# Optimization experiments

Hardware: AMD Instinct MI355X
Metric: run time of the kernel (lower is better)

The kernel has to match this reference:

```python
import jax, jax.numpy as jnp
import numpy as np

# Model hyperparameters (hardcoded in GarNetClassificationModel.__init__)
N_BLOCKS, N_AGG, N_FILT, N_PROP = 11, 4, 32, 20
B, V, F_IN = 128, 1024, 10
D_GEX = 2 * F_IN                                   # after GlobalExchange concat
D_UPD = N_FILT + N_AGG * 2 * (N_PROP + N_AGG) + N_AGG  # 32 + 192 + 4 = 228
BN_EPS = 1e-3                                      # keras BatchNormalization default


def setup_inputs() -> dict:
    key = jax.random.key(0)
    ks = iter(jax.random.split(key, 32))
    n = lambda shape, s=0.1: jax.random.normal(next(ks), shape, jnp.float32) * s
    return dict(
        x=jax.random.normal(next(ks), (B, V, F_IN), jnp.float32),
        bn0_gamma=jnp.ones((D_GEX,), jnp.float32),
        bn0_beta=jnp.zeros((D_GEX,), jnp.float32),
        bn0_mean=n((D_GEX,)),
        bn0_var=jax.random.uniform(next(ks), (D_GEX,), jnp.float32, 0.5, 1.5),
        W_in=n((D_GEX, N_FILT), 0.3),
        b_in=jnp.zeros((N_FILT,), jnp.float32),
        W_flr=n((N_BLOCKS, N_FILT, N_PROP), 0.2),
        b_flr=jnp.zeros((N_BLOCKS, N_PROP), jnp.float32),
        W_s=n((N_BLOCKS, N_FILT, N_AGG), 0.2),
        b_s=jnp.zeros((N_BLOCKS, N_AGG), jnp.float32),
        W_out=n((N_BLOCKS, D_UPD, N_FILT), 0.1),
        b_out=jnp.zeros((N_BLOCKS, N_FILT), jnp.float32),
        bn_gamma=jnp.ones((N_BLOCKS, N_FILT), jnp.float32),
        bn_beta=jnp.zeros((N_BLOCKS, N_FILT), jnp.float32),
        bn_mean=n((N_BLOCKS, N_FILT)),
        bn_var=jax.random.uniform(next(ks), (N_BLOCKS, N_FILT), jnp.float32, 0.5, 1.5),
        W_o0=n((N_BLOCKS * N_FILT, 48), 0.1),
        b_o0=jnp.zeros((48,), jnp.float32),
        W_o1=n((48, 3), 0.2),
        b_o1=jnp.zeros((3,), jnp.float32),
    )


def _bn(x, g, b, m, v):
    # inference-mode BatchNormalization over last axis
    return (x - m) * (g * jax.lax.rsqrt(v + BN_EPS)) + b


def reference(x, bn0_gamma, bn0_beta, bn0_mean, bn0_var, W_in, b_in,
              W_flr, b_flr, W_s, b_s, W_out, b_out,
              bn_gamma, bn_beta, bn_mean, bn_var,
              W_o0, b_o0, W_o1, b_o1):
    # GlobalExchange: concat per-event mean over vertices to each vertex
    mean = jnp.mean(x, axis=1, keepdims=True)                   # (B,1,F)
    h = jnp.concatenate([x, jnp.broadcast_to(mean, x.shape)], axis=-1)  # (B,V,2F)
    h = _bn(h, bn0_gamma, bn0_beta, bn0_mean, bn0_var)
    h = jnp.tanh(h @ W_in + b_in)                               # (B,V,32)

    def block(h, p):
        Wf, bf, Ws, bs, Wo, bo, g, be, m, v = p
        f = h @ Wf + bf                                  # (B,V,P) propagate features
        d = h @ Ws + bs                                  # (B,V,A) aggregator distances
        w = jnp.exp(-jnp.abs(d))                         # (B,V,A) edge weights
        feat = jnp.concatenate([f, w], axis=-1)          # (B,V,P+A)
        wf = w[..., None] * feat[:, :, None, :]          # (B,V,A,P+A)
        agg = jnp.concatenate([wf.max(axis=1), wf.mean(axis=1)], axis=-1)  # (B,A,2(P+A))
        upd = (w[..., None] * agg[:, None, :, :]).reshape(h.shape[0], h.shape[1], -1)  # (B,V,A*2(P+A))
        out = jnp.tanh(jnp.concatenate([h, upd, w], axis=-1) @ Wo + bo)  # (B,V,32)
        out = _bn(out, g, be, m, v)
        return out, out

    params = (W_flr, b_flr, W_s, b_s, W_out, b_out, bn_gamma, bn_beta, bn_mean, bn_var)
    _, feats = jax.lax.scan(block, h, params)            # feats: (L,B,V,32)
    feats = jnp.moveaxis(feats, 0, 2).reshape(x.shape[0], x.shape[1], -1)  # (B,V,L*32)

    h = jax.nn.relu(feats @ W_o0 + b_o0)                 # (B,V,48)
    return jax.nn.relu(h @ W_o1 + b_o1)                  # (B,V,3)
```

## Files before the change

### kernel.cpp

```cpp
#include <hip/hip_runtime.h>
#include <math.h>

#define NBLK  11
#define NAGG  4
#define NFILT 32
#define NPROP 20
#define BB    128
#define VV    1024
#define HV    512
#define FIN   10
#define TPB   512
#define BN_EPS 1e-3f
#define SHS   40

#define WSF_MEAN 128
#define WSF_AGG  (WSF_MEAN + BB*2*FIN)
#define WSF_FRAG (WSF_AGG + (BB*2*2) * NAGG * 48)
#define NFRAG    (NBLK*7*64*8)

typedef _Float16 f16;
typedef f16   f16x8 __attribute__((ext_vector_type(8)));
typedef float f32x4 __attribute__((ext_vector_type(4)));

__device__ __forceinline__ f32x4 MFMA(f16x8 a, f16x8 b, f32x4 c){
  return __builtin_amdgcn_mfma_f32_16x16x32_f16(a, b, c, 0, 0, 0);
}

__device__ __forceinline__ float fast_tanh(float x){
  float a = fabsf(x);
  float e = __expf(-2.0f * a);
  float r = (1.0f - e) / (1.0f + e);
  return copysignf(r, x);
}

__device__ __forceinline__ void pair_sync(int* flag, int target){
  __syncthreads();
  if (threadIdx.x == 0){
    asm volatile("s_waitcnt vmcnt(0)" ::: "memory");
    __hip_atomic_fetch_add(flag, 1, __ATOMIC_RELAXED, __HIP_MEMORY_SCOPE_AGENT);
    while (__hip_atomic_load(flag, __ATOMIC_RELAXED, __HIP_MEMORY_SCOPE_AGENT) < target)
      __builtin_amdgcn_s_sleep(2);
  }
  __syncthreads();
}

extern "C" __global__ void garnet_prep(
    const float* __restrict__ W_flr, const float* __restrict__ W_s,
    const float* __restrict__ W_out, const float* __restrict__ W_o0,
    f16* __restrict__ frag)
{
  const int idx = blockIdx.x * blockDim.x + threadIdx.x;
  if (idx >= NFRAG) return;
  const int j    = idx & 7;
  const int lane = (idx >> 3) & 63;
  const int rest = idx >> 9;
  const int set  = rest % 7;
  const int l    = rest / 7;
  const int l16  = lane & 15, kb = lane >> 4, k = kb*8 + j;
  float val = 0.f;
  if (set < 2){
    const int n = set*16 + l16;
    if (set == 0) val = W_flr[l*NFILT*NPROP + k*NPROP + n];
    else          val = (n < 20) ? W_flr[l*NFILT*NPROP + k*NPROP + n]
                       : (n < 24 ? W_s[l*NFILT*NAGG + k*NAGG + (n-20)] : 0.f);
  } else if (set < 4){
    const int s = set - 2;
    val = W_out[l*228*NFILT + k*NFILT + s*16 + l16];
  } else {
    const int s = set - 4;
    val = W_o0[((size_t)l*NFILT + k)*48 + s*16 + l16];
  }
  frag[idx] = (f16)val;
}

extern "C" __global__ __launch_bounds__(TPB)
void garnet_fused(
    const float* __restrict__ x,
    const float* __restrict__ bn0_g, const float* __restrict__ bn0_b,
    const float* __restrict__ bn0_m, const float* __restrict__ bn0_v,
    const float* __restrict__ W_in,  const float* __restrict__ b_in,
    const float* __restrict__ W_flr, const float* __restrict__ b_flr,
    const float* __restrict__ W_s,   const float* __restrict__ b_s,
    const float* __restrict__ W_out, const float* __restrict__ b_out,
    const float* __restrict__ bn_g,  const float* __restrict__ bn_b,
    const float* __restrict__ bn_m,  const float* __restrict__ bn_v,
    const float* __restrict__ W_o0,  const float* __restrict__ b_o0,
    const float* __restrict__ W_o1,  const float* __restrict__ b_o1,
    int* __restrict__ wsFlag, float* __restrict__ wsF,
    const f16* __restrict__ frag,
    float* __restrict__ out)
{
  const int wg   = blockIdx.x;
  const int b    = wg & (BB - 1);
  const int half = wg >> 7;
  const int t    = threadIdx.x;
  const int lane = t & 63;
  const int wave = t >> 6;
  const int v    = half * HV + t;
  const int l16  = lane & 15;
  const int kb   = lane >> 4;

  __shared__ float sFeat[HV * 25];
  __shared__ __align__(16) f16 sHhi[HV * SHS];
  __shared__ __align__(16) f16 sHlo[HV * SHS];
  __shared__ f16   sMh[4 * 32];
  __shared__ float sAgg[NAGG][48];
  __shared__ float sRed[8][FIN];
  __shared__ float sMean[FIN];

  int* flag = wsFlag + b;

  {
    float h[NFILT];
    float xv[FIN];
    const float* xp = x + ((size_t)b * VV + v) * FIN;
    #pragma unroll
    for (int c = 0; c < FIN; ++c) xv[c] = xp[c];

    float ps[FIN];
    #pragma unroll
    for (int c = 0; c < FIN; ++c) ps[c] = xv[c];
    #pragma unroll
    for (int m = 32; m > 0; m >>= 1){
      #pragma unroll
      for (int c = 0; c < FIN; ++c) ps[c] += __shfl_xor(ps[c], m, 64);
    }
    if (lane == 0){
      #pragma unroll
      for (int c = 0; c < FIN; ++c) sRed[wave][c] = ps[c];
    }
    __syncthreads();
    if (t < FIN){
      float s = 0.f;
      #pragma unroll
      for (int wv = 0; wv < 8; ++wv) s += sRed[wv][t];
      sRed[0][t] = s;
      __hip_atomic_store(&wsF[WSF_MEAN + (b*2 + half)*FIN + t], s,
                         __ATOMIC_RELAXED, __HIP_MEMORY_SCOPE_AGENT);
    }
    pair_sync(flag, 2);
    if (t < FIN){
      float theirs = __hip_atomic_load(&wsF[WSF_MEAN + (b*2 + (half^1))*FIN + t],
                                       __ATOMIC_RELAXED, __HIP_MEMORY_SCOPE_AGENT);
      sMean[t] = (sRed[0][t] + theirs) * (1.0f / VV);
    }
    __syncthreads();

    float o[NFILT];
    #pragma unroll
    for (int j = 0; j < NFILT; ++j) o[j] = b_in[j];
    #pragma unroll
    for (int c = 0; c < FIN; ++c){
      const float zx = (xv[c]    - bn0_m[c])     * (bn0_g[c]     * rsqrtf(bn0_v[c]     + BN_EPS)) + bn0_b[c];
      const float zm = (sMean[c] - bn0_m[FIN+c]) * (bn0_g[FIN+c] * rsqrtf(bn0_v[FIN+c] + BN_EPS)) + bn0_b[FIN+c];
      #pragma unroll
      for (int j = 0; j < NFILT; ++j)
        o[j] += zx * W_in[c*NFILT + j] + zm * W_in[(FIN+c)*NFILT + j];
    }
    #pragma unroll
    for (int j = 0; j < NFILT; ++j) h[j] = fast_tanh(o[j]);

    #pragma unroll
    for (int c = 0; c < 4; ++c){
      f16x8 hh, hl;
      #pragma unroll
      for (int j = 0; j < 8; ++j){
        const float hv = h[c*8 + j];
        const f16 a = (f16)hv;
        hh[j] = a;
        hl[j] = (f16)(hv - (float)a);
      }
      *(f16x8*)&sHhi[t*SHS + c*8] = hh;
      *(f16x8*)&sHlo[t*SHS + c*8] = hl;
    }
  }
  __syncthreads();

  f32x4 acc[4][3];
  #pragma unroll
  for (int s = 0; s < 3; ++s){
    const float a0 = b_o0[s*16 + l16];
    #pragma unroll
    for (int i = 0; i < 4; ++i) acc[i][s] = (f32x4){a0, a0, a0, a0};
  }

  for (int l = 0; l < NBLK; ++l){
    const float* Wf = W_flr + l * NFILT * NPROP;
    const float* bf = b_flr + l * NPROP;
    const float* Ws = W_s   + l * NFILT * NAGG;
    const float* bs = b_s   + l * NAGG;
    const float* Wo = W_out + l * 228 * NFILT;
    const float* bo = b_out + l * NFILT;
    const float* g_ = bn_g  + l * NFILT;
    const float* be = bn_b  + l * NFILT;
    const float* bm = bn_m  + l * NFILT;
    const float* bv = bn_v  + l * NFILT;
    const f16*  fl  = frag + (size_t)l * 7 * 64 * 8;

    {
      f16x8 b1f0, b1f1;
      if (frag){
        b1f0 = *(const f16x8*)&fl[(size_t)(0*64 + lane)*8];
        b1f1 = *(const f16x8*)&fl[(size_t)(1*64 + lane)*8];
      } else {
        #pragma unroll
        for (int j = 0; j < 8; ++j){
          const int k = kb*8 + j;
          b1f0[j] = (f16)Wf[k*NPROP + l16];
          const int n = 16 + l16;
          b1f1[j] = (f16)((n < 20) ? Wf[k*NPROP + n] : (n < 24 ? Ws[k*NAGG + (n-20)] : 0.f));
        }
      }
      const float bias0 = bf[l16];
      const int  c1 = 16 + l16;
      const float bias1 = (c1 < 20) ? bf[c1] : (c1 < 24 ? bs[c1-20] : 0.f);

      #pragma unroll
      for (int i = 0; i < 4; ++i){
        const int tb = wave*64 + i*16;
        const f16x8 ahi = *(const f16x8*)&sHhi[(tb + l16)*SHS + kb*8];
        const f16x8 alo = *(const f16x8*)&sHlo[(tb + l16)*SHS + kb*8];
        f32x4 c0 = (f32x4){bias0, bias0, bias0, bias0};
        c0 = MFMA(ahi, b1f0, c0);
        c0 = MFMA(alo, b1f0, c0);
        #pragma unroll
        for (int q = 0; q < 4; ++q)
          sFeat[(tb + kb*4 + q)*25 + l16] = c0[q];
        f32x4 c1v = (f32x4){bias1, bias1, bias1, bias1};
        c1v = MFMA(ahi, b1f1, c1v);
        c1v = MFMA(alo, b1f1, c1v);
        if (l16 < 4){
          #pragma unroll
          for (int q = 0; q < 4; ++q)
            sFeat[(tb + kb*4 + q)*25 + 16 + l16] = c1v[q];
        } else if (l16 < 8){
          #pragma unroll
          for (int q = 0; q < 4; ++q)
            sFeat[(tb + kb*4 + q)*25 + 16 + l16] = __expf(-fabsf(c1v[q]));
        }
      }
    }
    __syncthreads();

    {
      const int w3 = wave * 3;
      float psum[NAGG][3], pmax[NAGG][3];
      #pragma unroll
      for (int a = 0; a < NAGG; ++a)
        #pragma unroll
        for (int c = 0; c < 3; ++c){ psum[a][c] = 0.f; pmax[a][c] = -INFINITY; }
      for (int i = 0; i < 8; ++i){
        const int row = i * 64 + lane;
        float fc[3], wa[NAGG];
        #pragma unroll
        for (int c = 0; c < 3; ++c) fc[c] = sFeat[row*25 + w3 + c];
        #pragma unroll
        for (int a = 0; a < NAGG; ++a) wa[a] = sFeat[row*25 + NPROP + a];
        #pragma unroll
        for (int a = 0; a < NAGG; ++a)
          #pragma unroll
          for (int c = 0; c < 3; ++c){
            const float p = wa[a] * fc[c];
            psum[a][c] += p;
            pmax[a][c]  = fmaxf(pmax[a][c], p);
          }
      }
      #pragma unroll
      for (int m = 32; m > 0; m >>= 1){
        #pragma unroll
        for (int a = 0; a < NAGG; ++a)
          #pragma unroll
          for (int c = 0; c < 3; ++c){
            psum[a][c] += __shfl_xor(psum[a][c], m, 64);
            pmax[a][c]  = fmaxf(pmax[a][c], __shfl_xor(pmax[a][c], m, 64));
          }
      }
      if (lane == 0){
        float* gp = wsF + WSF_AGG + (((size_t)(b*2 + (l&1))*2 + half) * NAGG * 48);
        #pragma unroll
        for (int a = 0; a < NAGG; ++a)
          #pragma unroll
          for (int c = 0; c < 3; ++c){
            sAgg[a][w3 + c]      = pmax[a][c];
            sAgg[a][24 + w3 + c] = psum[a][c];
            __hip_atomic_store(&gp[a*48 + w3 + c],      pmax[a][c], __ATOMIC_RELAXED, __HIP_MEMORY_SCOPE_AGENT);
            __hip_atomic_store(&gp[a*48 + 24 + w3 + c], psum[a][c], __ATOMIC_RELAXED, __HIP_MEMORY_SCOPE_AGENT);
          }
      }
    }
    pair_sync(flag, 2*l + 4);

    if (t < 192){
      const int a = t / 48, c = t - a * 48;
      const float* pp = wsF + WSF_AGG + (((size_t)(b*2 + (l&1))*2 + (half^1)) * NAGG * 48);
      const float mine   = sAgg[a][c];
      const float theirs = __hip_atomic_load(&pp[a*48 + c], __ATOMIC_RELAXED, __HIP_MEMORY_SCOPE_AGENT);
      sAgg[a][c] = (c < 24) ? fmaxf(mine, theirs) : (mine + theirs) * (1.0f / VV);
    }
    __syncthreads();

    if (t < 128){
      const int a = t >> 5, j = t & 31;
      float m = Wo[(224 + a) * NFILT + j];
      #pragma unroll 8
      for (int c = 0; c < 48; ++c) m += sAgg[a][c] * Wo[(32 + a*48 + c) * NFILT + j];
      sMh[a*32 + j] = (f16)m;
    }
    __syncthreads();

    {
      f16x8 b2f0, b2f1;
      if (frag){
        b2f0 = *(const f16x8*)&fl[(size_t)(2*64 + lane)*8];
        b2f1 = *(const f16x8*)&fl[(size_t)(3*64 + lane)*8];
      } else {
        #pragma unroll
        for (int j = 0; j < 8; ++j){
          const int k = kb*8 + j;
          b2f0[j] = (f16)Wo[k*NFILT + l16];
          b2f1[j] = (f16)Wo[k*NFILT + 16 + l16];
        }
      }
      f16x8 bmf[2];
      #pragma unroll
      for (int s = 0; s < 2; ++s)
        #pragma unroll
        for (int j = 0; j < 8; ++j)
          bmf[s][j] = (kb == 0 && j < 4) ? sMh[j*32 + s*16 + l16] : (f16)0.f;

      float boc[2], bmc[2], scc[2], bec[2];
      #pragma unroll
      for (int s = 0; s < 2; ++s){
        const int cc = s*16 + l16;
        boc[s] = bo[cc];
        bmc[s] = bm[cc];
        scc[s] = g_[cc] * rsqrtf(bv[cc] + BN_EPS);
        bec[s] = be[cc];
      }

      #pragma unroll
      for (int i = 0; i < 4; ++i){
        const int tb = wave*64 + i*16;
        const f16x8 ahi = *(const f16x8*)&sHhi[(tb + l16)*SHS + kb*8];
        const f16x8 alo = *(const f16x8*)&sHlo[(tb + l16)*SHS + kb*8];
        f16x8 wa;
        #pragma unroll
        for (int j = 0; j < 8; ++j) wa[j] = (f16)0.f;
        {
          const float w0 = sFeat[(tb + l16)*25 + 20];
          const float w1 = sFeat[(tb + l16)*25 + 21];
          const float w2 = sFeat[(tb + l16)*25 + 22];
          const float w3v = sFeat[(tb + l16)*25 + 23];
          if (kb == 0){ wa[0]=(f16)w0; wa[1]=(f16)w1; wa[2]=(f16)w2; wa[3]=(f16)w3v; }
        }
        #pragma unroll
        for (int s = 0; s < 2; ++s){
          f32x4 o = (f32x4){0.f, 0.f, 0.f, 0.f};
          o = MFMA(ahi, (s ? b2f1 : b2f0), o);
          o = MFMA(alo, (s ? b2f1 : b2f0), o);
          o = MFMA(wa,  bmf[s], o);
          #pragma unroll
          for (int q = 0; q < 4; ++q){
            const float th = fast_tanh(o[q] + boc[s]);
            const float hn = (th - bmc[s]) * scc[s] + bec[s];
            const f16 hh = (f16)hn;
            const int idx = (tb + kb*4 + q)*SHS + s*16 + l16;
            sHhi[idx] = hh;
            sHlo[idx] = (f16)(hn - (float)hh);
          }
        }
      }
    }
    asm volatile("s_waitcnt lgkmcnt(0)" ::: "memory");

    {
      f16x8 b3f[3];
      if (frag){
        #pragma unroll
        for (int s = 0; s < 3; ++s)
          b3f[s] = *(const f16x8*)&fl[(size_t)((4 + s)*64 + lane)*8];
      } else {
        const float* Wo0l = W_o0 + (size_t)l * NFILT * 48;
        #pragma unroll
        for (int s = 0; s < 3; ++s)
          #pragma unroll
          for (int j = 0; j < 8; ++j)
            b3f[s][j] = (f16)Wo0l[(kb*8 + j)*48 + s*16 + l16];
      }
      #pragma unroll
      for (int i = 0; i < 4; ++i){
        const int tb = wave*64 + i*16;
        const f16x8 ahi = *(const f16x8*)&sHhi[(tb + l16)*SHS + kb*8];
        const f16x8 alo = *(const f16x8*)&sHlo[(tb + l16)*SHS + kb*8];
        #pragma unroll
        for (int s = 0; s < 3; ++s){
          acc[i][s] = MFMA(ahi, b3f[s], acc[i][s]);
          acc[i][s] = MFMA(alo, b3f[s], acc[i][s]);
        }
      }
    }
  }

  {
    float w1c[3][3];
    #pragma unroll
    for (int s = 0; s < 3; ++s)
      #pragma unroll
      for (int m = 0; m < 3; ++m) w1c[s][m] = W_o1[(s*16 + l16)*3 + m];
    const float bo1_0 = b_o1[0], bo1_1 = b_o1[1], bo1_2 = b_o1[2];

    #pragma unroll
    for (int i = 0; i < 4; ++i){
      const int tb = wave*64 + i*16;
      float p[4][3];
      #pragma unroll
      for (int q = 0; q < 4; ++q){ p[q][0]=0.f; p[q][1]=0.f; p[q][2]=0.f; }
      #pragma unroll
      for (int s = 0; s < 3; ++s)
        #pragma unroll
        for (int q = 0; q < 4; ++q){
          const float r_ = fmaxf(acc[i][s][q], 0.f);
          p[q][0] += r_ * w1c[s][0];
          p[q][1] += r_ * w1c[s][1];
          p[q][2] += r_ * w1c[s][2];
        }
      #pragma unroll
      for (int m = 1; m <= 8; m <<= 1)
        #pragma unroll
        for (int q = 0; q < 4; ++q){
          p[q][0] += __shfl_xor(p[q][0], m, 64);
          p[q][1] += __shfl_xor(p[q][1], m, 64);
          p[q][2] += __shfl_xor(p[q][2], m, 64);
        }
      if (l16 < 3){
        const float bo1v = (l16 == 0) ? bo1_0 : ((l16 == 1) ? bo1_1 : bo1_2);
        #pragma unroll
        for (int q = 0; q < 4; ++q){
          const float vv = (l16 == 0) ? p[q][0] : ((l16 == 1) ? p[q][1] : p[q][2]);
          out[((size_t)b*VV + half*HV + tb + kb*4 + q)*3 + l16] = fmaxf(vv + bo1v, 0.f);
        }
      }
    }
  }
}

extern "C" void kernel_launch(void* const* d_in, const int* in_sizes, int n_in,
                              void* d_out, int out_size, void* d_ws, size_t ws_size,
                              hipStream_t stream) {
  const float* x      = (const float*)d_in[0];
  const float* bn0_g  = (const float*)d_in[1];
  const float* bn0_b  = (const float*)d_in[2];
  const float* bn0_m  = (const float*)d_in[3];
  const float* bn0_v  = (const float*)d_in[4];
  const float* W_in   = (const float*)d_in[5];
  const float* b_in   = (const float*)d_in[6];
  const float* W_flr  = (const float*)d_in[7];
  const float* b_flr  = (const float*)d_in[8];
  const float* W_s    = (const float*)d_in[9];
  const float* b_s    = (const float*)d_in[10];
  const float* W_out  = (const float*)d_in[11];
  const float* b_out  = (const float*)d_in[12];
  const float* bn_g   = (const float*)d_in[13];
  const float* bn_b   = (const float*)d_in[14];
  const float* bn_m   = (const float*)d_in[15];
  const float* bn_v   = (const float*)d_in[16];
  const float* W_o0   = (const float*)d_in[17];
  const float* b_o0   = (const float*)d_in[18];
  const float* W_o1   = (const float*)d_in[19];
  const float* b_o1   = (const float*)d_in[20];

  float* wsF = (float*)d_ws;
  const size_t needed = (size_t)WSF_FRAG * 4 + (size_t)NFRAG * 2;
  _Float16* frag = (ws_size >= needed) ? (_Float16*)(wsF + WSF_FRAG) : nullptr;

  hipMemsetAsync(d_ws, 0, BB * sizeof(int), stream);

  if (frag)
    garnet_prep<<<dim3((NFRAG + 255) / 256), dim3(256), 0, stream>>>(
        W_flr, W_s, W_out, W_o0, frag);

  garnet_fused<<<dim3(BB * 2), dim3(TPB), 0, stream>>>(
      x, bn0_g, bn0_b, bn0_m, bn0_v, W_in, b_in,
      W_flr, b_flr, W_s, b_s, W_out, b_out,
      bn_g, bn_b, bn_m, bn_v, W_o0, b_o0, W_o1, b_o1,
      (int*)d_ws, wsF, frag, (float*)d_out);
}
```

Baseline: 164.1 us.

## Overlap previous block's output projection with cross-workgroup sync wait; transpose feature buffer

The per-block W_o0 accumulation (phaseC) for layer l-1 is deferred and run between the atomic flag increment and the spin-wait on the partner workgroup, so the MFMA work hides the inter-workgroup barrier latency. The final layer's accumulation moves after the loop. The sFeat buffer is also transposed to a feature-major layout with padded stride, enabling vectorized f32x4 stores and conflict-free column reads. This relies on sHhi/sHlo still holding layer l-1's hidden state during the wait, which holds because the update phase runs after the sync.

```diff
diff --git a/kernel.cpp b/kernel.cpp
--- a/kernel.cpp
+++ b/kernel.cpp
@@ -12,6 +12,7 @@
 #define TPB   512
 #define BN_EPS 1e-3f
 #define SHS   40
+#define SFS   536
 
 #define WSF_MEAN 128
 #define WSF_AGG  (WSF_MEAN + BB*2*FIN)
@@ -31,17 +32,6 @@
   float e = __expf(-2.0f * a);
   float r = (1.0f - e) / (1.0f + e);
   return copysignf(r, x);
-}
-
-__device__ __forceinline__ void pair_sync(int* flag, int target){
-  __syncthreads();
-  if (threadIdx.x == 0){
-    asm volatile("s_waitcnt vmcnt(0)" ::: "memory");
-    __hip_atomic_fetch_add(flag, 1, __ATOMIC_RELAXED, __HIP_MEMORY_SCOPE_AGENT);
-    while (__hip_atomic_load(flag, __ATOMIC_RELAXED, __HIP_MEMORY_SCOPE_AGENT) < target)
-      __builtin_amdgcn_s_sleep(2);
-  }
-  __syncthreads();
 }
 
 extern "C" __global__ void garnet_prep(
@@ -100,7 +90,7 @@
   const int l16  = lane & 15;
   const int kb   = lane >> 4;
 
-  __shared__ float sFeat[HV * 25];
+  __shared__ float sFeatT[24 * SFS];
   __shared__ __align__(16) f16 sHhi[HV * SHS];
   __shared__ __align__(16) f16 sHlo[HV * SHS];
   __shared__ f16   sMh[4 * 32];
@@ -110,6 +100,36 @@
 
   int* flag = wsFlag + b;
 
+  f32x4 acc[4][3];
+
+  auto phaseC = [&](int lc){
+    f16x8 b3f[3];
+    if (frag){
+      const f16* flC = frag + (size_t)lc * 7 * 64 * 8;
+      #pragma unroll
+      for (int s = 0; s < 3; ++s)
+        b3f[s] = *(const f16x8*)&flC[(size_t)((4 + s)*64 + lane)*8];
+    } else {
+      const float* Wo0l = W_o0 + (size_t)lc * NFILT * 48;
+      #pragma unroll
+      for (int s = 0; s < 3; ++s)
+        #pragma unroll
+        for (int j = 0; j < 8; ++j)
+          b3f[s][j] = (f16)Wo0l[(kb*8 + j)*48 + s*16 + l16];
+    }
+    #pragma unroll
+    for (int i = 0; i < 4; ++i){
+      const int tb = wave*64 + i*16;
+      const f16x8 ahi = *(const f16x8*)&sHhi[(tb + l16)*SHS + kb*8];
+      const f16x8 alo = *(const f16x8*)&sHlo[(tb + l16)*SHS + kb*8];
+      #pragma unroll
+      for (int s = 0; s < 3; ++s){
+        acc[i][s] = MFMA(ahi, b3f[s], acc[i][s]);
+        acc[i][s] = MFMA(alo, b3f[s], acc[i][s]);
+      }
+    }
+  };
+
   {
     float h[NFILT];
     float xv[FIN];
@@ -138,7 +158,14 @@
       __hip_atomic_store(&wsF[WSF_MEAN + (b*2 + half)*FIN + t], s,
                          __ATOMIC_RELAXED, __HIP_MEMORY_SCOPE_AGENT);
     }
-    pair_sync(flag, 2);
+    __syncthreads();
+    if (t == 0){
+      asm volatile("s_waitcnt vmcnt(0)" ::: "memory");
+      __hip_atomic_fetch_add(flag, 1, __ATOMIC_RELAXED, __HIP_MEMORY_SCOPE_AGENT);
+      while (__hip_atomic_load(flag, __ATOMIC_RELAXED, __HIP_MEMORY_SCOPE_AGENT) < 2)
+        __builtin_amdgcn_s_sleep(2);
+    }
+    __syncthreads();
     if (t < FIN){
       float theirs = __hip_atomic_load(&wsF[WSF_MEAN + (b*2 + (half^1))*FIN + t],
                                        __ATOMIC_RELAXED, __HIP_MEMORY_SCOPE_AGENT);
@@ -176,7 +203,6 @@
   }
   __syncthreads();
 
-  f32x4 acc[4][3];
   #pragma unroll
   for (int s = 0; s < 3; ++s){
     const float a0 = b_o0[s*16 + l16];
@@ -223,20 +249,17 @@
         f32x4 c0 = (f32x4){bias0, bias0, bias0, bias0};
         c0 = MFMA(ahi, b1f0, c0);
         c0 = MFMA(alo, b1f0, c0);
-        #pragma unroll
-        for (int q = 0; q < 4; ++q)
-          sFeat[(tb + kb*4 + q)*25 + l16] = c0[q];
+        *(f32x4*)&sFeatT[l16*SFS + tb + kb*4] = c0;
         f32x4 c1v = (f32x4){bias1, bias1, bias1, bias1};
         c1v = MFMA(ahi, b1f1, c1v);
         c1v = MFMA(alo, b1f1, c1v);
         if (l16 < 4){
+          *(f32x4*)&sFeatT[(16 + l16)*SFS + tb + kb*4] = c1v;
+        } else if (l16 < 8){
+          f32x4 e;
           #pragma unroll
-          for (int q = 0; q < 4; ++q)
-            sFeat[(tb + kb*4 + q)*25 + 16 + l16] = c1v[q];
-        } else if (l16 < 8){
-          #pragma unroll
-          for (int q = 0; q < 4; ++q)
-            sFeat[(tb + kb*4 + q)*25 + 16 + l16] = __expf(-fabsf(c1v[q]));
+          for (int q = 0; q < 4; ++q) e[q] = __expf(-fabsf(c1v[q]));
+          *(f32x4*)&sFeatT[(16 + l16)*SFS + tb + kb*4] = e;
         }
       }
     }
@@ -253,9 +276,9 @@
         const int row = i * 64 + lane;
         float fc[3], wa[NAGG];
         #pragma unroll
-        for (int c = 0; c < 3; ++c) fc[c] = sFeat[row*25 + w3 + c];
-        #pragma unroll
-        for (int a = 0; a < NAGG; ++a) wa[a] = sFeat[row*25 + NPROP + a];
+        for (int c = 0; c < 3; ++c) fc[c] = sFeatT[(w3 + c)*SFS + row];
+        #pragma unroll
+        for (int a = 0; a < NAGG; ++a) wa[a] = sFeatT[(20 + a)*SFS + row];
         #pragma unroll
         for (int a = 0; a < NAGG; ++a)
           #pragma unroll
@@ -288,7 +311,19 @@
           }
       }
     }
-    pair_sync(flag, 2*l + 4);
+    __syncthreads();
+
+    if (t == 0){
+      asm volatile("s_waitcnt vmcnt(0)" ::: "memory");
+      __hip_atomic_fetch_add(flag, 1, __ATOMIC_RELAXED, __HIP_MEMORY_SCOPE_AGENT);
+    }
+    __builtin_amdgcn_sched_barrier(0);
+    if (l > 0) phaseC(l - 1);
+    if (t == 0){
+      while (__hip_atomic_load(flag, __ATOMIC_RELAXED, __HIP_MEMORY_SCOPE_AGENT) < 2*l + 4)
+        __builtin_amdgcn_s_sleep(2);
+    }
+    __syncthreads();
 
     if (t < 192){
       const int a = t / 48, c = t - a * 48;
@@ -347,10 +382,10 @@
         #pragma unroll
         for (int j = 0; j < 8; ++j) wa[j] = (f16)0.f;
         {
-          const float w0 = sFeat[(tb + l16)*25 + 20];
-          const float w1 = sFeat[(tb + l16)*25 + 21];
-          const float w2 = sFeat[(tb + l16)*25 + 22];
-          const float w3v = sFeat[(tb + l16)*25 + 23];
+          const float w0 = sFeatT[20*SFS + tb + l16];
+          const float w1 = sFeatT[21*SFS + tb + l16];
+          const float w2 = sFeatT[22*SFS + tb + l16];
+          const float w3v = sFeatT[23*SFS + tb + l16];
           if (kb == 0){ wa[0]=(f16)w0; wa[1]=(f16)w1; wa[2]=(f16)w2; wa[3]=(f16)w3v; }
         }
         #pragma unroll
@@ -372,34 +407,9 @@
       }
     }
     asm volatile("s_waitcnt lgkmcnt(0)" ::: "memory");
-
-    {
-      f16x8 b3f[3];
-      if (frag){
-        #pragma unroll
-        for (int s = 0; s < 3; ++s)
-          b3f[s] = *(const f16x8*)&fl[(size_t)((4 + s)*64 + lane)*8];
-      } else {
-        const float* Wo0l = W_o0 + (size_t)l * NFILT * 48;
-        #pragma unroll
-        for (int s = 0; s < 3; ++s)
-          #pragma unroll
-          for (int j = 0; j < 8; ++j)
-            b3f[s][j] = (f16)Wo0l[(kb*8 + j)*48 + s*16 + l16];
-      }
-      #pragma unroll
-      for (int i = 0; i < 4; ++i){
-        const int tb = wave*64 + i*16;
-        const f16x8 ahi = *(const f16x8*)&sHhi[(tb + l16)*SHS + kb*8];
-        const f16x8 alo = *(const f16x8*)&sHlo[(tb + l16)*SHS + kb*8];
-        #pragma unroll
-        for (int s = 0; s < 3; ++s){
-          acc[i][s] = MFMA(ahi, b3f[s], acc[i][s]);
-          acc[i][s] = MFMA(alo, b3f[s], acc[i][s]);
-        }
-      }
-    }
   }
+
+  phaseC(NBLK - 1);
 
   {
     float w1c[3][3];
```

Measured after the change: 164.7 us. Within noise of the previous version (+0.4%).
